# Kernel optimization log

Measured on AMD Instinct MI355X. Metric: run time of the kernel, lower is better.

Reference implementation:

```python
import jax, jax.numpy as jnp
import numpy as np

K = 5  # kernel_size


def _unfold(x, k):
    """Torch F.unfold equivalent: [B,C,H,W] -> [B,C,k*k,H,W].
    Patch index is row-major over the kxk window (dy*k+dx), matching
    F.unfold's channel-major / window-row-major layout after view(B,C,k*k,H,W)."""
    p = k // 2
    B, C, H, W = x.shape
    xp = jnp.pad(x, ((0, 0), (0, 0), (p, p), (p, p)))
    patches = [xp[:, :, dy:dy + H, dx:dx + W] for dy in range(k) for dx in range(k)]
    return jnp.stack(patches, axis=2)


def _conv2d(x, w, b, pad):
    y = jax.lax.conv_general_dilated(
        x, w, window_strides=(1, 1), padding=[(pad, pad), (pad, pad)],
        dimension_numbers=("NCHW", "OIHW", "NCHW"))
    return y + b[None, :, None, None]


def setup_inputs() -> dict:
    key = jax.random.key(0)
    k0, k1, k2 = jax.random.split(key, 3)
    B, H, W = 2, 1024, 1024
    flow = jax.random.normal(k0, (B, 2, H, W), jnp.float32)
    # kernel_gen params: Conv2d(3,32,3,pad=1) -> ReLU -> Conv2d(32,50,1)
    w1 = jax.random.normal(k1, (32, 3, 3, 3), jnp.float32) * 0.1
    b1 = jnp.zeros((32,), jnp.float32)
    w2 = jax.random.normal(k2, (K * K * 2, 32, 1, 1), jnp.float32) * 0.1
    b2 = jnp.zeros((K * K * 2,), jnp.float32)
    return {"flow": flow, "w1": w1, "b1": b1, "w2": w2, "b2": b2}


def reference(flow, w1, b1, w2, b2):
    B, _, H, W = flow.shape
    patches = _unfold(flow, K)                       # [B,2,25,H,W]
    # torch .var(dim=2) defaults to unbiased (ddof=1)
    var = jnp.var(patches, axis=2, ddof=1)           # [B,2,H,W]
    consistency = jnp.exp(-jnp.sqrt(jnp.sum(var * var, axis=1, keepdims=True)))  # [B,1,H,W]
    guidance = jnp.concatenate([flow, consistency], axis=1)  # [B,3,H,W]
    h = jax.nn.relu(_conv2d(guidance, w1, b1, pad=1))        # [B,32,H,W]
    kernels = _conv2d(h, w2, b2, pad=0).reshape(B, 2, K * K, H, W)
    refined = jnp.sum(kernels * patches, axis=2)             # [B,2,H,W]
    return refined
```

## Files before the change

### kernel.cpp

```cpp
#include <hip/hip_runtime.h>
#include <math.h>

#define KSZ 5
#define TS 16
#define HALO 3
#define FW (TS + 2*HALO)
#define FWP (FW + 1)
#define CW (TS + 2)
#define SF_C (FW*FWP)
#define SC_BASE (2*SF_C)
#define SMF_TOT (SC_BASE + 18*FWP)

typedef __attribute__((ext_vector_type(8))) short short8_t;
typedef __attribute__((ext_vector_type(4))) float float4_t;
typedef __attribute__((ext_vector_type(2))) unsigned int uint2_t;

static __device__ __forceinline__ unsigned short f2bf(float f) {
    union { float f; unsigned int u; } v; v.f = f;
    return (unsigned short)((v.u + 0x7FFFu + ((v.u >> 16) & 1u)) >> 16);
}
static __device__ __forceinline__ unsigned int pk2t(float a, float b) {
    union { float f; unsigned int u; } ua, ub; ua.f = a; ub.f = b;
    return __builtin_amdgcn_perm(ub.u, ua.u, 0x07060302u);
}

static __device__ __forceinline__ void slot_decode(int n, int& c, int& sel, int& idx, bool& valid) {
    int g4c = (n >> 2) & 3;
    c = g4c >> 1; sel = g4c & 1;
    idx = ((n >> 4) << 2) + (n & 3);
    valid = sel ? (idx < 10) : (idx < 15);
}

static __device__ __forceinline__ int kperm(int s) {
    int sg = s >> 3, sj = s & 7;
    if (sg < 3) return sg*9 + sj;
    if (sj == 1) return 8;
    if (sj == 2) return 17;
    if (sj == 4) return 26;
    return -1;
}

__global__ __launch_bounds__(256)
void pack_kernel(const float* __restrict__ w1, const float* __restrict__ b1,
                 const float* __restrict__ w2, const float* __restrict__ b2,
                 unsigned short* __restrict__ wp, float* __restrict__ bp)
{
    const int tid = threadIdx.x;
    for (int i = tid; i < 6*64*8; i += 256) {
        int f = i >> 9, l = (i >> 3) & 63, j = i & 7;
        int m = l & 15, s = ((l >> 4) << 3) + j;
        float v;
        if (f < 2) {
            int k = kperm(s);
            v = (k >= 0) ? w1[(f*16 + m)*27 + k] : 0.f;
        } else {
            int n = (f - 2)*16 + m;
            int c, sel, idx; bool valid;
            slot_decode(n, c, sel, idx, valid);
            v = valid ? w2[(c*25 + sel*15 + idx)*32 + s] : 0.f;
        }
        wp[i] = f2bf(v);
    }
    for (int i = tid; i < 6*64*4; i += 256) {
        int f = i >> 8, l = (i >> 2) & 63, r = i & 3, g4 = l >> 4;
        float v;
        if (f < 2) v = b1[f*16 + g4*4 + r];
        else {
            int n = (f - 2)*16 + g4*4 + r;
            int c, sel, idx; bool valid;
            slot_decode(n, c, sel, idx, valid);
            v = valid ? b2[c*25 + sel*15 + idx] : 0.f;
        }
        bp[i] = v;
    }
}

__global__ __launch_bounds__(256)
void refine_kernel(const float* __restrict__ flow,
                   const unsigned short* __restrict__ wp,
                   const float* __restrict__ bp,
                   float* __restrict__ out, int H, int W)
{
    __shared__ float smf[SMF_TOT];
    __shared__ __align__(16) char dyn[6400];

    const int tid = threadIdx.x;
    const int x0 = blockIdx.x * TS;
    const int y0 = blockIdx.y * TS;
    const int b  = blockIdx.z;

    const int lane = tid & 63;
    const int wave = tid >> 6;
    const int col  = lane & 15;
    const int g4   = lane >> 4;
    const int key  = col >> 2;

    short8_t w1A[2], w2A[4];
    float4_t cb1[2], cb2[4];
    #pragma unroll
    for (int nt = 0; nt < 2; ++nt) {
        w1A[nt] = *(const short8_t*)&wp[(nt*64 + lane)*8];
        cb1[nt] = *(const float4_t*)&bp[(nt*64 + lane)*4];
    }
    #pragma unroll
    for (int nt = 0; nt < 4; ++nt) {
        w2A[nt] = *(const short8_t*)&wp[((2+nt)*64 + lane)*8];
        cb2[nt] = *(const float4_t*)&bp[((2+nt)*64 + lane)*4];
    }

    for (int c = 0; c < 2; ++c) {
        const float* src = flow + ((size_t)(b*2+c) * H) * W;
        for (int i = tid; i < FW*FW; i += 256) {
            int ly = i / FW, lx = i - ly*FW;
            int gy = y0 - HALO + ly, gx = x0 - HALO + lx;
            float v = 0.f;
            if (gy >= 0 && gy < H && gx >= 0 && gx < W) v = src[(size_t)gy*W + gx];
            smf[c*SF_C + ly*FWP + lx] = v;
        }
    }
    __syncthreads();

    {
        float4_t* rs = (float4_t*)dyn;
        if (tid < FW*(CW/2)) {
            int y = tid / (CW/2), xp = (tid - y*(CW/2)) * 2;
            const float* r0 = &smf[y*FWP + xp];
            const float* r1 = &smf[SF_C + y*FWP + xp];
            float a0=r0[0], a1=r0[1], a2=r0[2], a3=r0[3], a4=r0[4], a5=r0[5];
            float c0=r1[0], c1=r1[1], c2=r1[2], c3=r1[3], c4=r1[4], c5=r1[5];
            float sA = ((a0+a1)+(a2+a3))+a4;
            float qA = fmaf(a4,a4, fmaf(a3,a3, fmaf(a2,a2, fmaf(a1,a1, a0*a0))));
            float sB = ((c0+c1)+(c2+c3))+c4;
            float qB = fmaf(c4,c4, fmaf(c3,c3, fmaf(c2,c2, fmaf(c1,c1, c0*c0))));
            float sA1 = sA + a5 - a0;
            float qA1 = fmaf(-a0, a0, fmaf(a5, a5, qA));
            float sB1 = sB + c5 - c0;
            float qB1 = fmaf(-c0, c0, fmaf(c5, c5, qB));
            rs[y*CW + xp]     = (float4_t){sA,  qA,  sB,  qB };
            rs[y*CW + xp + 1] = (float4_t){sA1, qA1, sB1, qB1};
        }
    }
    __syncthreads();

    for (int i = tid; i < CW*CW; i += 256) {
        int py = i / CW, px = i - py*CW;
        int gy = y0 - 1 + py, gx = x0 - 1 + px;
        float cons = 0.f;
        if (gy >= 0 && gy < H && gx >= 0 && gx < W) {
            const float4_t* rp = (const float4_t*)dyn + py*CW + px;
            float4_t acc = rp[0];
            #pragma unroll
            for (int dy = 1; dy < KSZ; ++dy) acc += rp[dy*CW];
            float v0 = (acc.y - acc.x*acc.x*(1.f/25.f)) * (1.f/24.f);
            float v1 = (acc.w - acc.z*acc.z*(1.f/25.f)) * (1.f/24.f);
            cons = __expf(-sqrtf(v0*v0 + v1*v1));
        }
        smf[SC_BASE + py*FWP + px] = cons;
    }
    __syncthreads();

    unsigned short* hb = (unsigned short*)dyn;

    int gb0, gb1, gb2, gb3;
    {
        int ty0 = wave*4;
        int p0 = 0*SF_C + (ty0 + 2)*FWP + (col + 2);
        int p1 = 1*SF_C + (ty0 + 2)*FWP + (col + 2);
        int p2 = SC_BASE + ty0*FWP + col;
        if (g4 == 0)      { gb0 = gb1 = gb2 = gb3 = p0; }
        else if (g4 == 1) { gb0 = gb1 = gb2 = gb3 = p1; }
        else if (g4 == 2) { gb0 = gb1 = gb2 = gb3 = p2; }
        else { gb0 = p0 + 47; gb1 = p1 + 46; gb2 = p2 + 24; gb3 = p0; }
    }

    const int sel = g4 & 1, pc = g4 >> 1;
    int pb = pc*SF_C + sel*(3*FWP) + FWP + 1 + col + (wave*4)*FWP;
    float pv[15];
    #pragma unroll
    for (int i = 0; i < 15; ++i) pv[i] = smf[pb + (i/5)*FWP + (i%5)];

    const int hrow = (wave*16 + col) * 64;
    const int hw0 = hrow + (((0*2 + (g4 >> 1)) ^ key) << 4) + ((g4 & 1) << 3);
    const int hw1 = hrow + (((1*2 + (g4 >> 1)) ^ key) << 4) + ((g4 & 1) << 3);
    const int hro = hrow + ((g4 ^ key) << 4);

    #pragma unroll
    for (int mt = 0; mt < 4; ++mt) {
        const int ty = wave*4 + mt;

        float ga = smf[gb0 + 0],  gbv = smf[gb0 + 1];
        float gc = smf[gb1 + 2],  gd  = smf[gb1 + 23];
        float ge = smf[gb2 + 24], gf  = smf[gb2 + 25];
        float gg = smf[gb3 + 46], gh  = smf[gb3 + 47];
        union { unsigned int u[4]; short8_t s; } gu;
        gu.u[0] = pk2t(ga, gbv); gu.u[1] = pk2t(gc, gd);
        gu.u[2] = pk2t(ge, gf);  gu.u[3] = pk2t(gg, gh);
        short8_t gB = gu.s;
        gb0 += FWP; gb1 += FWP; gb2 += FWP; gb3 += FWP;

        float4_t h0 = __builtin_amdgcn_mfma_f32_16x16x32_bf16(w1A[0], gB, cb1[0], 0, 0, 0);
        float4_t h1 = __builtin_amdgcn_mfma_f32_16x16x32_bf16(w1A[1], gB, cb1[1], 0, 0, 0);

        {
            uint2_t d0, d1;
            d0.x = pk2t(fmaxf(h0[0],0.f), fmaxf(h0[1],0.f));
            d0.y = pk2t(fmaxf(h0[2],0.f), fmaxf(h0[3],0.f));
            d1.x = pk2t(fmaxf(h1[0],0.f), fmaxf(h1[1],0.f));
            d1.y = pk2t(fmaxf(h1[2],0.f), fmaxf(h1[3],0.f));
            *(uint2_t*)((char*)hb + hw0) = d0;
            *(uint2_t*)((char*)hb + hw1) = d1;
        }
        short8_t hf = *(const short8_t*)((char*)hb + hro);

        float4_t ka[4];
        #pragma unroll
        for (int nt = 0; nt < 4; ++nt)
            ka[nt] = __builtin_amdgcn_mfma_f32_16x16x32_bf16(w2A[nt], hf, cb2[nt], 0, 0, 0);

        float s = 0.f;
        #pragma unroll
        for (int i = 0; i < 15; ++i)
            s = fmaf(ka[i >> 2][i & 3], pv[i], s);

        if (mt < 3) {
            #pragma unroll
            for (int i = 0; i < 10; ++i) pv[i] = pv[i + 5];
            pb += FWP;
            #pragma unroll
            for (int i = 10; i < 15; ++i) pv[i] = smf[pb + (i/5)*FWP + (i%5)];
        }

        s += __shfl_xor(s, 16);

        if ((g4 & 1) == 0) {
            int y = y0 + ty, x = x0 + col;
            out[((size_t)(b*2 + pc) * H + y) * W + x] = s;
        }
    }
}

extern "C" void kernel_launch(void* const* d_in, const int* in_sizes, int n_in,
                              void* d_out, int out_size, void* d_ws, size_t ws_size,
                              hipStream_t stream) {
    const float* flow = (const float*)d_in[0];
    const float* w1   = (const float*)d_in[1];
    const float* b1   = (const float*)d_in[2];
    const float* w2   = (const float*)d_in[3];
    const float* b2   = (const float*)d_in[4];
    float* out = (float*)d_out;

    unsigned short* wp = (unsigned short*)d_ws;
    float* bp = (float*)((char*)d_ws + 8192);

    const int H = 1024, W = 1024;
    const int B = in_sizes[0] / (2 * H * W);

    pack_kernel<<<1, 256, 0, stream>>>(w1, b1, w2, b2, wp, bp);
    dim3 grid(W / TS, H / TS, B);
    refine_kernel<<<grid, dim3(256), 0, stream>>>(flow, wp, bp, out, H, W);
}
```

Before: 126.1 us.

## Enlarge tile to 16x32 and add fast interior path for halo loads

Doubles the tile height so each block computes 32 rows, with each wave handling 8 rows instead of 4. This lowers the halo overhead per output pixel and halves the block count. It also adds a branch that skips bounds checks for interior tiles and merges both channel loads into one loop. The cost is more LDS per block, which may reduce occupancy, and longer per-wave serial work.

```diff
diff --git a/kernel.cpp b/kernel.cpp
--- a/kernel.cpp
+++ b/kernel.cpp
@@ -2,14 +2,15 @@
 #include <math.h>
 
 #define KSZ 5
-#define TS 16
+#define TSX 16
+#define TSY 32
 #define HALO 3
-#define FW (TS + 2*HALO)
-#define FWP (FW + 1)
-#define CW (TS + 2)
-#define SF_C (FW*FWP)
+#define FWX 22
+#define FH  38
+#define PITCH 23
+#define SF_C (FH*PITCH)
 #define SC_BASE (2*SF_C)
-#define SMF_TOT (SC_BASE + 18*FWP)
+#define SMF_TOT (SC_BASE + 34*PITCH)
 
 typedef __attribute__((ext_vector_type(8))) short short8_t;
 typedef __attribute__((ext_vector_type(4))) float float4_t;
@@ -82,11 +83,11 @@
                    float* __restrict__ out, int H, int W)
 {
     __shared__ float smf[SMF_TOT];
-    __shared__ __align__(16) char dyn[6400];
+    __shared__ __align__(16) char dyn[10960];
 
     const int tid = threadIdx.x;
-    const int x0 = blockIdx.x * TS;
-    const int y0 = blockIdx.y * TS;
+    const int x0 = blockIdx.x * TSX;
+    const int y0 = blockIdx.y * TSY;
     const int b  = blockIdx.z;
 
     const int lane = tid & 63;
@@ -108,24 +109,37 @@
         cb2[nt] = *(const float4_t*)&bp[((2+nt)*64 + lane)*4];
     }
 
-    for (int c = 0; c < 2; ++c) {
-        const float* src = flow + ((size_t)(b*2+c) * H) * W;
-        for (int i = tid; i < FW*FW; i += 256) {
-            int ly = i / FW, lx = i - ly*FW;
-            int gy = y0 - HALO + ly, gx = x0 - HALO + lx;
-            float v = 0.f;
-            if (gy >= 0 && gy < H && gx >= 0 && gx < W) v = src[(size_t)gy*W + gx];
-            smf[c*SF_C + ly*FWP + lx] = v;
+    {
+        const float* srcb = flow + (size_t)(b*2) * H * W;
+        if (x0 >= HALO && x0 + TSX + HALO <= W && y0 >= HALO && y0 + TSY + HALO <= H) {
+            const float* s = srcb + (size_t)(y0 - HALO) * W + (x0 - HALO);
+            for (int i = tid; i < 2*FH*FWX; i += 256) {
+                int c = 0, r = i;
+                if (r >= FH*FWX) { c = 1; r -= FH*FWX; }
+                int ly = r / FWX, lx = r - ly*FWX;
+                smf[c*SF_C + ly*PITCH + lx] = s[(size_t)c*H*W + ly*W + lx];
+            }
+        } else {
+            for (int i = tid; i < 2*FH*FWX; i += 256) {
+                int c = 0, r = i;
+                if (r >= FH*FWX) { c = 1; r -= FH*FWX; }
+                int ly = r / FWX, lx = r - ly*FWX;
+                int gy = y0 - HALO + ly, gx = x0 - HALO + lx;
+                float v = 0.f;
+                if (gy >= 0 && gy < H && gx >= 0 && gx < W)
+                    v = srcb[(size_t)c*H*W + (size_t)gy*W + gx];
+                smf[c*SF_C + ly*PITCH + lx] = v;
+            }
         }
     }
     __syncthreads();
 
     {
         float4_t* rs = (float4_t*)dyn;
-        if (tid < FW*(CW/2)) {
-            int y = tid / (CW/2), xp = (tid - y*(CW/2)) * 2;
-            const float* r0 = &smf[y*FWP + xp];
-            const float* r1 = &smf[SF_C + y*FWP + xp];
+        for (int i = tid; i < FH*9; i += 256) {
+            int y = i / 9, xp = (i - y*9) * 2;
+            const float* r0 = &smf[y*PITCH + xp];
+            const float* r1 = &smf[SF_C + y*PITCH + xp];
             float a0=r0[0], a1=r0[1], a2=r0[2], a3=r0[3], a4=r0[4], a5=r0[5];
             float c0=r1[0], c1=r1[1], c2=r1[2], c3=r1[3], c4=r1[4], c5=r1[5];
             float sA = ((a0+a1)+(a2+a3))+a4;
@@ -136,26 +150,26 @@
             float qA1 = fmaf(-a0, a0, fmaf(a5, a5, qA));
             float sB1 = sB + c5 - c0;
             float qB1 = fmaf(-c0, c0, fmaf(c5, c5, qB));
-            rs[y*CW + xp]     = (float4_t){sA,  qA,  sB,  qB };
-            rs[y*CW + xp + 1] = (float4_t){sA1, qA1, sB1, qB1};
+            rs[y*18 + xp]     = (float4_t){sA,  qA,  sB,  qB };
+            rs[y*18 + xp + 1] = (float4_t){sA1, qA1, sB1, qB1};
         }
     }
     __syncthreads();
 
-    for (int i = tid; i < CW*CW; i += 256) {
-        int py = i / CW, px = i - py*CW;
+    for (int i = tid; i < 34*18; i += 256) {
+        int py = i / 18, px = i - py*18;
         int gy = y0 - 1 + py, gx = x0 - 1 + px;
         float cons = 0.f;
         if (gy >= 0 && gy < H && gx >= 0 && gx < W) {
-            const float4_t* rp = (const float4_t*)dyn + py*CW + px;
+            const float4_t* rp = (const float4_t*)dyn + py*18 + px;
             float4_t acc = rp[0];
             #pragma unroll
-            for (int dy = 1; dy < KSZ; ++dy) acc += rp[dy*CW];
+            for (int dy = 1; dy < KSZ; ++dy) acc += rp[dy*18];
             float v0 = (acc.y - acc.x*acc.x*(1.f/25.f)) * (1.f/24.f);
             float v1 = (acc.w - acc.z*acc.z*(1.f/25.f)) * (1.f/24.f);
             cons = __expf(-sqrtf(v0*v0 + v1*v1));
         }
-        smf[SC_BASE + py*FWP + px] = cons;
+        smf[SC_BASE + py*PITCH + px] = cons;
     }
     __syncthreads();
 
@@ -163,10 +177,10 @@
 
     int gb0, gb1, gb2, gb3;
     {
-        int ty0 = wave*4;
-        int p0 = 0*SF_C + (ty0 + 2)*FWP + (col + 2);
-        int p1 = 1*SF_C + (ty0 + 2)*FWP + (col + 2);
-        int p2 = SC_BASE + ty0*FWP + col;
+        int ty0 = wave*8;
+        int p0 = 0*SF_C + (ty0 + 2)*PITCH + (col + 2);
+        int p1 = 1*SF_C + (ty0 + 2)*PITCH + (col + 2);
+        int p2 = SC_BASE + ty0*PITCH + col;
         if (g4 == 0)      { gb0 = gb1 = gb2 = gb3 = p0; }
         else if (g4 == 1) { gb0 = gb1 = gb2 = gb3 = p1; }
         else if (g4 == 2) { gb0 = gb1 = gb2 = gb3 = p2; }
@@ -174,19 +188,19 @@
     }
 
     const int sel = g4 & 1, pc = g4 >> 1;
-    int pb = pc*SF_C + sel*(3*FWP) + FWP + 1 + col + (wave*4)*FWP;
+    int pb = pc*SF_C + sel*(3*PITCH) + PITCH + 1 + col + (wave*8)*PITCH;
     float pv[15];
     #pragma unroll
-    for (int i = 0; i < 15; ++i) pv[i] = smf[pb + (i/5)*FWP + (i%5)];
+    for (int i = 0; i < 15; ++i) pv[i] = smf[pb + (i/5)*PITCH + (i%5)];
 
     const int hrow = (wave*16 + col) * 64;
-    const int hw0 = hrow + (((0*2 + (g4 >> 1)) ^ key) << 4) + ((g4 & 1) << 3);
-    const int hw1 = hrow + (((1*2 + (g4 >> 1)) ^ key) << 4) + ((g4 & 1) << 3);
+    const int hw0 = hrow + (((0*2 + pc) ^ key) << 4) + (sel << 3);
+    const int hw1 = hrow + (((1*2 + pc) ^ key) << 4) + (sel << 3);
     const int hro = hrow + ((g4 ^ key) << 4);
 
     #pragma unroll
-    for (int mt = 0; mt < 4; ++mt) {
-        const int ty = wave*4 + mt;
+    for (int mt = 0; mt < 8; ++mt) {
+        const int ty = wave*8 + mt;
 
         float ga = smf[gb0 + 0],  gbv = smf[gb0 + 1];
         float gc = smf[gb1 + 2],  gd  = smf[gb1 + 23];
@@ -196,7 +210,7 @@
         gu.u[0] = pk2t(ga, gbv); gu.u[1] = pk2t(gc, gd);
         gu.u[2] = pk2t(ge, gf);  gu.u[3] = pk2t(gg, gh);
         short8_t gB = gu.s;
-        gb0 += FWP; gb1 += FWP; gb2 += FWP; gb3 += FWP;
+        gb0 += PITCH; gb1 += PITCH; gb2 += PITCH; gb3 += PITCH;
 
         float4_t h0 = __builtin_amdgcn_mfma_f32_16x16x32_bf16(w1A[0], gB, cb1[0], 0, 0, 0);
         float4_t h1 = __builtin_amdgcn_mfma_f32_16x16x32_bf16(w1A[1], gB, cb1[1], 0, 0, 0);
@@ -222,17 +236,17 @@
         for (int i = 0; i < 15; ++i)
             s = fmaf(ka[i >> 2][i & 3], pv[i], s);
 
-        if (mt < 3) {
+        if (mt < 7) {
             #pragma unroll
             for (int i = 0; i < 10; ++i) pv[i] = pv[i + 5];
-            pb += FWP;
+            pb += PITCH;
             #pragma unroll
-            for (int i = 10; i < 15; ++i) pv[i] = smf[pb + (i/5)*FWP + (i%5)];
+            for (int i = 10; i < 15; ++i) pv[i] = smf[pb + (i/5)*PITCH + (i%5)];
         }
 
         s += __shfl_xor(s, 16);
 
-        if ((g4 & 1) == 0) {
+        if (sel == 0) {
             int y = y0 + ty, x = x0 + col;
             out[((size_t)(b*2 + pc) * H + y) * W + x] = s;
         }
@@ -256,6 +270,6 @@
     const int B = in_sizes[0] / (2 * H * W);
 
     pack_kernel<<<1, 256, 0, stream>>>(w1, b1, w2, b2, wp, bp);
-    dim3 grid(W / TS, H / TS, B);
+    dim3 grid(W / TSX, H / TSY, B);
     refine_kernel<<<grid, dim3(256), 0, stream>>>(flow, wp, bp, out, H, W);
 }
```

Result: faster. 118.7 us (-5.9%).
